# Performance work log

Hardware: AMD Instinct MI355X
Metric: run time of the kernel (lower is better)

The kernel has to match this reference:

```python
import jax, jax.numpy as jnp
import numpy as np


def _patches3x3(x):
    # x: [B,H,W,C] -> [B,H,W,9,C], SAME zero padding, patch index k = i*3+j
    B, H, W, C = x.shape
    p = jnp.pad(x, ((0, 0), (1, 1), (1, 1), (0, 0)))
    return jnp.stack([p[:, i:i + H, j:j + W, :] for i in range(3) for j in range(3)], axis=3)


def setup_inputs() -> dict:
    key = jax.random.key(0)
    k1, k2, k3 = jax.random.split(key, 3)
    B, H, W, CH, NC, DIM = 4, 80, 80, 256, 22, 256
    x = jax.random.normal(k1, (B, H, W, CH), dtype=jnp.float32)
    seg_mask = jax.random.uniform(k2, (B, H, W, NC), dtype=jnp.float32)
    # he_uniform over receptive field ch*3*3
    lim = np.sqrt(6.0 / (CH * 9)).astype(np.float32)
    conv_w = jax.random.uniform(k3, (CH, 3, 3, DIM), dtype=jnp.float32, minval=-lim, maxval=lim)
    return {"x": x, "seg_mask": seg_mask, "conv_w": conv_w}


def reference(x, seg_mask, conv_w):
    B, H, W, CH = x.shape
    NC = seg_mask.shape[-1]
    DIM = conv_w.shape[-1]
    # patches of segmentation map: [B,H,W,9,NC]
    s_patch = _patches3x3(seg_mask)
    m = seg_mask[:, :, :, None, :]                       # [B,H,W,1,NC]
    s_max = jnp.max(m, axis=-1, keepdims=True)           # [B,H,W,1,1]
    # keep patch values only for the argmax class at the center pixel
    sel = jnp.sum(jnp.where(m == s_max, s_patch, 0.0), axis=-1)  # [B,H,W,9]
    cnt = jnp.sum((sel != 0.0).astype(jnp.float32), axis=-1, keepdims=True)  # [B,H,W,1]
    norm = jnp.where(cnt > 0, 9.0 / jnp.maximum(cnt, 1.0), 0.0)  # divide_no_nan(9, cnt)
    # per-channel 3x3 patch extraction of features (== depthwise conv with eye(9))
    xp = _patches3x3(x)                                  # [B,H,W,9,CH]
    xp = xp * sel[..., None]                             # mask-gated patches
    w = conv_w.reshape(CH, 9, DIM)
    out = jnp.einsum('bhwkc,ckd->bhwd', xp, w) * norm    # [B,H,W,DIM]
    return out
```

## Files before the change

### kernel.cpp

```cpp
#include <hip/hip_runtime.h>
#include <hip/hip_bf16.h>
#include <cstdint>

#define B_ 4
#define H_ 80
#define W_ 80
#define CH_ 256
#define NC_ 22
#define DIM_ 256
#define NPIX (B_*H_*W_)

typedef __attribute__((ext_vector_type(8))) short short8;
typedef __attribute__((ext_vector_type(4))) float floatx4;

static __device__ inline unsigned short f2bf(float v) {
    __hip_bfloat16 h = __float2bfloat16(v);
    unsigned short r;
    __builtin_memcpy(&r, &h, 2);
    return r;
}

__global__ __launch_bounds__(256) void sel_kernel(const float* __restrict__ seg,
                                                  float* __restrict__ ssel)
{
    int m = blockIdx.x * 256 + threadIdx.x;
    if (m >= NPIX) return;
    int w = m % W_;
    int h = (m / W_) % H_;
    int b = m / (W_ * H_);

    const float2* c2 = (const float2*)(seg + (size_t)m * NC_);
    float cv[NC_];
    #pragma unroll
    for (int c = 0; c < NC_ / 2; ++c) { float2 v = c2[c]; cv[2*c] = v.x; cv[2*c+1] = v.y; }
    float mx = -1e30f;
    #pragma unroll
    for (int c = 0; c < NC_; ++c) mx = fmaxf(mx, cv[c]);

    float sel[9];
    int cnt = 0;
    #pragma unroll
    for (int k = 0; k < 9; ++k) {
        int i = k / 3, j = k % 3;
        int hh = h + i - 1, ww = w + j - 1;
        float s = 0.f;
        if (hh >= 0 && hh < H_ && ww >= 0 && ww < W_) {
            const float2* n2 = (const float2*)(seg + ((size_t)((b * H_ + hh) * W_ + ww)) * NC_);
            #pragma unroll
            for (int c = 0; c < NC_ / 2; ++c) {
                float2 v = n2[c];
                s += (cv[2*c]   == mx) ? v.x : 0.f;
                s += (cv[2*c+1] == mx) ? v.y : 0.f;
            }
        }
        sel[k] = s;
        cnt += (s != 0.f) ? 1 : 0;
    }
    float norm = (cnt > 0) ? 9.f / (float)cnt : 0.f;
    #pragma unroll
    for (int k = 0; k < 9; ++k)
        ssel[k * NPIX + m] = sel[k] * norm;
}

__global__ __launch_bounds__(256) void cvt_w_kernel(const float* __restrict__ cw,
                                                    unsigned short* __restrict__ wbT)
{
    int t = blockIdx.x * 256 + threadIdx.x;
    if (t >= 9 * 256 * 32) return;
    int c8 = t & 31;
    int d  = (t >> 5) & 255;
    int k  = t >> 13;
    unsigned int u[4];
    #pragma unroll
    for (int e = 0; e < 4; ++e) {
        float v0 = cw[(size_t)(c8*8 + 2*e    ) * 9 * DIM_ + k * DIM_ + d];
        float v1 = cw[(size_t)(c8*8 + 2*e + 1) * 9 * DIM_ + k * DIM_ + d];
        u[e] = (unsigned)f2bf(v0) | ((unsigned)f2bf(v1) << 16);
    }
    uint4* dst = (uint4*)(wbT + ((size_t)k * 256 + d) * 256 + c8 * 8);
    *dst = make_uint4(u[0], u[1], u[2], u[3]);
}

__global__ __launch_bounds__(256, 3) void conv_mfma(const float* __restrict__ x,
                                                    const float* __restrict__ ssel,
                                                    const unsigned short* __restrict__ wbT,
                                                    float* __restrict__ out)
{
    __shared__ __align__(16) unsigned short xsc[2][80][40];
    __shared__ __align__(16) unsigned short wl[2][128][40];
    __shared__ float sl[9][80];

    const int tid  = threadIdx.x;
    const int lane = tid & 63;
    const int wv   = tid >> 6;
    const int ln   = lane & 15;
    const int quad = lane >> 4;
    const int rt   = blockIdx.x;
    const int b    = rt / H_;
    const int h    = rt % H_;
    const int d0   = blockIdx.y * 128;

    const bool xact = tid < 160;
    const int  xtm  = tid >> 1;
    const int  xth  = tid & 1;
    const int  wtd  = tid >> 1;
    const int  wth  = tid & 1;

    for (int t = tid; t < 9 * 80; t += 256) {
        int k = t / 80, m = t - k * 80;
        sl[k][m] = ssel[k * NPIX + rt * W_ + m];
    }
    __syncthreads();

    floatx4 acc[5][2];
    #pragma unroll
    for (int i = 0; i < 5; ++i)
        #pragma unroll
        for (int j = 0; j < 2; ++j)
            acc[i][j] = (floatx4){0.f, 0.f, 0.f, 0.f};

    float4 xr0, xr1, xr2, xr3;
    float4 wr0, wr1;
    float  sc = 0.f;
    bool   xnz = false;

    auto stage1 = [&](int it) {
        const int k2  = it % 9;
        const int cc2 = (it / 9) * 32;
        const int i2  = k2 / 3;
        const int j2  = k2 - 3 * i2;
        const float4* q = (const float4*)(wbT + (((size_t)k2 * 256 + d0 + wtd) * 256
                                                 + cc2 + wth * 16));
        wr0 = q[0];
        wr1 = q[1];
        if (xact) {
            sc = sl[k2][xtm];
            const int r = h + i2 - 1;
            const int c = xtm + j2 - 1;
            xnz = (r >= 0) && (r < H_) && (c >= 0) && (c < W_);
            if (xnz) {
                const float4* p = (const float4*)(x + ((((size_t)b * H_ + r) * W_ + c) * CH_
                                                       + cc2 + xth * 16));
                xr0 = p[0]; xr1 = p[1]; xr2 = p[2]; xr3 = p[3];
            }
        }
    };

    auto stage2 = [&](int it) {
        const int buf = it & 1;
        float4* wd = (float4*)&wl[buf][wtd][wth * 16];
        wd[0] = wr0;
        wd[1] = wr1;
        if (xact) {
            unsigned int u[8];
            if (xnz) {
                float f[16] = {xr0.x, xr0.y, xr0.z, xr0.w, xr1.x, xr1.y, xr1.z, xr1.w,
                               xr2.x, xr2.y, xr2.z, xr2.w, xr3.x, xr3.y, xr3.z, xr3.w};
                #pragma unroll
                for (int e = 0; e < 8; ++e)
                    u[e] = (unsigned)f2bf(f[2*e] * sc) | ((unsigned)f2bf(f[2*e+1] * sc) << 16);
            } else {
                #pragma unroll
                for (int e = 0; e < 8; ++e) u[e] = 0u;
            }
            uint4* xd = (uint4*)&xsc[buf][xtm][xth * 16];
            xd[0] = make_uint4(u[0], u[1], u[2], u[3]);
            xd[1] = make_uint4(u[4], u[5], u[6], u[7]);
        }
    };

    stage1(0);
    stage2(0);
    __syncthreads();

    for (int it = 0; it < 72; ++it) {
        const int nit = it + 1;
        if (nit < 72) stage1(nit);

        const int buf = it & 1;
        short8 a[5];
        #pragma unroll
        for (int i = 0; i < 5; ++i)
            a[i] = *(const short8*)&xsc[buf][i * 16 + ln][quad * 8];
        short8 bb[2];
        #pragma unroll
        for (int j = 0; j < 2; ++j)
            bb[j] = *(const short8*)&wl[buf][wv * 32 + j * 16 + ln][quad * 8];
        #pragma unroll
        for (int i = 0; i < 5; ++i)
            #pragma unroll
            for (int j = 0; j < 2; ++j)
                acc[i][j] = __builtin_amdgcn_mfma_f32_16x16x32_bf16(a[i], bb[j], acc[i][j],
                                                                    0, 0, 0);

        if (nit < 72) stage2(nit);
        __syncthreads();
    }

    #pragma unroll
    for (int i = 0; i < 5; ++i) {
        #pragma unroll
        for (int j = 0; j < 2; ++j) {
            const int dd = d0 + wv * 32 + j * 16 + ln;
            #pragma unroll
            for (int r = 0; r < 4; ++r) {
                const int m = i * 16 + quad * 4 + r;
                out[((size_t)(rt * W_ + m)) * DIM_ + dd] = acc[i][j][r];
            }
        }
    }
}

extern "C" void kernel_launch(void* const* d_in, const int* in_sizes, int n_in,
                              void* d_out, int out_size, void* d_ws, size_t ws_size,
                              hipStream_t stream)
{
    const float* x   = (const float*)d_in[0];
    const float* seg = (const float*)d_in[1];
    const float* cw  = (const float*)d_in[2];
    float* out = (float*)d_out;

    float*          ssel = (float*)d_ws;
    unsigned short* wbT  = (unsigned short*)((char*)d_ws + 921600);

    sel_kernel<<<dim3((NPIX + 255) / 256), dim3(256), 0, stream>>>(seg, ssel);
    cvt_w_kernel<<<dim3(288), dim3(256), 0, stream>>>(cw, wbT);
    conv_mfma<<<dim3(B_ * H_, DIM_ / 128), dim3(256), 0, stream>>>(x, ssel, wbT, out);
}
```

Before: 173.6 us.

## Restructure conv GEMM with 128-channel K tiles, register B, and bf16 x precast

```diff
diff --git a/kernel.cpp b/kernel.cpp
--- a/kernel.cpp
+++ b/kernel.cpp
@@ -10,20 +10,24 @@
 #define DIM_ 256
 #define NPIX (B_*H_*W_)
 
+typedef unsigned short ushort;
 typedef __attribute__((ext_vector_type(8))) short short8;
 typedef __attribute__((ext_vector_type(4))) float floatx4;
 
-static __device__ inline unsigned short f2bf(float v) {
+static __device__ inline ushort f2bf(float v) {
     __hip_bfloat16 h = __float2bfloat16(v);
-    unsigned short r;
+    ushort r;
     __builtin_memcpy(&r, &h, 2);
     return r;
 }
-
-__global__ __launch_bounds__(256) void sel_kernel(const float* __restrict__ seg,
-                                                  float* __restrict__ ssel)
-{
-    int m = blockIdx.x * 256 + threadIdx.x;
+static __device__ inline unsigned pk2(float a, float b) {
+    return (unsigned)f2bf(a) | ((unsigned)f2bf(b) << 16);
+}
+
+__global__ __launch_bounds__(64) void sel_kernel(const float* __restrict__ seg,
+                                                 float* __restrict__ ssel)
+{
+    int m = blockIdx.x * 64 + threadIdx.x;
     if (m >= NPIX) return;
     int w = m % W_;
     int h = (m / W_) % H_;
@@ -62,33 +66,54 @@
         ssel[k * NPIX + m] = sel[k] * norm;
 }
 
-__global__ __launch_bounds__(256) void cvt_w_kernel(const float* __restrict__ cw,
-                                                    unsigned short* __restrict__ wbT)
-{
-    int t = blockIdx.x * 256 + threadIdx.x;
-    if (t >= 9 * 256 * 32) return;
-    int c8 = t & 31;
-    int d  = (t >> 5) & 255;
-    int k  = t >> 13;
-    unsigned int u[4];
-    #pragma unroll
-    for (int e = 0; e < 4; ++e) {
-        float v0 = cw[(size_t)(c8*8 + 2*e    ) * 9 * DIM_ + k * DIM_ + d];
-        float v1 = cw[(size_t)(c8*8 + 2*e + 1) * 9 * DIM_ + k * DIM_ + d];
-        u[e] = (unsigned)f2bf(v0) | ((unsigned)f2bf(v1) << 16);
-    }
-    uint4* dst = (uint4*)(wbT + ((size_t)k * 256 + d) * 256 + c8 * 8);
-    *dst = make_uint4(u[0], u[1], u[2], u[3]);
-}
-
-__global__ __launch_bounds__(256, 3) void conv_mfma(const float* __restrict__ x,
-                                                    const float* __restrict__ ssel,
-                                                    const unsigned short* __restrict__ wbT,
-                                                    float* __restrict__ out)
-{
-    __shared__ __align__(16) unsigned short xsc[2][80][40];
-    __shared__ __align__(16) unsigned short wl[2][128][40];
-    __shared__ float sl[9][80];
+__global__ __launch_bounds__(256) void cvt_w(const float* __restrict__ cw,
+                                             ushort* __restrict__ wbT)
+{
+    __shared__ ushort ls[32][260];
+    const int k  = blockIdx.x / 8;
+    const int c0 = (blockIdx.x % 8) * 32;
+    const int c   = threadIdx.x >> 3;
+    const int seg = threadIdx.x & 7;
+
+    const float* src = cw + ((size_t)(c0 + c) * 9 + k) * DIM_ + seg * 32;
+    #pragma unroll
+    for (int e = 0; e < 32; e += 4) {
+        float4 v = *(const float4*)(src + e);
+        unsigned* dst = (unsigned*)&ls[c][seg * 32 + e];
+        dst[0] = pk2(v.x, v.y);
+        dst[1] = pk2(v.z, v.w);
+    }
+    __syncthreads();
+
+    const int d = threadIdx.x;
+    ushort tmp[32];
+    #pragma unroll
+    for (int cc = 0; cc < 32; ++cc) tmp[cc] = ls[cc][d];
+    uint4 o[4];
+    __builtin_memcpy(o, tmp, 64);
+    uint4* dst = (uint4*)(wbT + ((size_t)k * 256 + d) * 256 + c0);
+    dst[0] = o[0]; dst[1] = o[1]; dst[2] = o[2]; dst[3] = o[3];
+}
+
+__global__ __launch_bounds__(256) void cvt_x(const float* __restrict__ x,
+                                             ushort* __restrict__ xb)
+{
+    size_t idx = ((size_t)blockIdx.x * 256 + threadIdx.x) * 8;
+    const float4* s = (const float4*)(x + idx);
+    float4 a = s[0], b = s[1];
+    uint4 o = make_uint4(pk2(a.x, a.y), pk2(a.z, a.w), pk2(b.x, b.y), pk2(b.z, b.w));
+    *(uint4*)(xb + idx) = o;
+}
+
+template<bool XB16>
+__global__ __launch_bounds__(256, 3) void conv2(const float* __restrict__ x,
+                                                const ushort* __restrict__ xb,
+                                                const float* __restrict__ ssel,
+                                                const ushort* __restrict__ wbT,
+                                                float* __restrict__ out)
+{
+    __shared__ ushort xsA[2][80 * 136];
+    __shared__ float  sl[9][80];
 
     const int tid  = threadIdx.x;
     const int lane = tid & 63;
@@ -100,112 +125,147 @@
     const int h    = rt % H_;
     const int d0   = blockIdx.y * 128;
 
-    const bool xact = tid < 160;
-    const int  xtm  = tid >> 1;
-    const int  xth  = tid & 1;
-    const int  wtd  = tid >> 1;
-    const int  wth  = tid & 1;
+    int qm[5], qc[5];
+    #pragma unroll
+    for (int r = 0; r < 5; ++r) {
+        int q = tid + 256 * r;
+        qm[r] = q >> 4;
+        qc[r] = q & 15;
+    }
 
     for (int t = tid; t < 9 * 80; t += 256) {
         int k = t / 80, m = t - k * 80;
         sl[k][m] = ssel[k * NPIX + rt * W_ + m];
     }
+
+    floatx4 O[5][2];
+    #pragma unroll
+    for (int i = 0; i < 5; ++i)
+        #pragma unroll
+        for (int jn = 0; jn < 2; ++jn)
+            O[i][jn] = (floatx4){0.f, 0.f, 0.f, 0.f};
+
+    uint4  sg[5];
+    float4 fa[5], fb[5];
+    bool   ok[5];
+
+    auto stage_load = [&](int nit) {
+        const int i   = nit / 6;
+        const int rem = nit % 6;
+        const int cc  = (rem / 3) * 128;
+        const int jj  = rem % 3;
+        const int rr  = h + i - 1;
+        const bool rowok = (rr >= 0) && (rr < H_);
+        const int rsafe = rowok ? rr : h;
+        #pragma unroll
+        for (int r = 0; r < 5; ++r) {
+            const int col = qm[r] + jj - 1;
+            const bool v = rowok && (col >= 0) && (col < W_);
+            ok[r] = v;
+            const size_t gp = ((size_t)(b * H_ + rsafe) * W_ + (v ? col : 0));
+            if (XB16) {
+                sg[r] = *(const uint4*)(xb + gp * CH_ + cc + qc[r] * 8);
+            } else {
+                const float* f = x + gp * CH_ + cc + qc[r] * 8;
+                fa[r] = *(const float4*)f;
+                fb[r] = *(const float4*)(f + 4);
+            }
+        }
+    };
+    auto stage_write = [&](int nit) {
+        ushort* bp = xsA[nit & 1];
+        #pragma unroll
+        for (int r = 0; r < 5; ++r) {
+            uint4 v;
+            if (XB16) {
+                v = ok[r] ? sg[r] : make_uint4(0u, 0u, 0u, 0u);
+            } else {
+                v = ok[r] ? make_uint4(pk2(fa[r].x, fa[r].y), pk2(fa[r].z, fa[r].w),
+                                       pk2(fb[r].x, fb[r].y), pk2(fb[r].z, fb[r].w))
+                          : make_uint4(0u, 0u, 0u, 0u);
+            }
+            *(uint4*)&bp[qm[r] * 136 + qc[r] * 8] = v;
+        }
+    };
+
+    short8 Breg[8];
+    auto loadB = [&](int nit) {
+        const int i   = nit / 6;
+        const int rem = nit % 6;
+        const int cc  = (rem / 3) * 128;
+        const int jj  = rem % 3;
+        const int k   = 3 * i + jj;
+        #pragma unroll
+        for (int kk = 0; kk < 4; ++kk)
+            #pragma unroll
+            for (int jn = 0; jn < 2; ++jn)
+                Breg[kk * 2 + jn] = *(const short8*)(wbT
+                    + ((size_t)k * 256 + d0 + wv * 32 + jn * 16 + ln) * 256
+                    + cc + kk * 32 + quad * 8);
+    };
+
+    stage_load(0);
+    stage_write(0);
+    loadB(0);
     __syncthreads();
 
-    floatx4 acc[5][2];
-    #pragma unroll
-    for (int i = 0; i < 5; ++i)
-        #pragma unroll
-        for (int j = 0; j < 2; ++j)
-            acc[i][j] = (floatx4){0.f, 0.f, 0.f, 0.f};
-
-    float4 xr0, xr1, xr2, xr3;
-    float4 wr0, wr1;
-    float  sc = 0.f;
-    bool   xnz = false;
-
-    auto stage1 = [&](int it) {
-        const int k2  = it % 9;
-        const int cc2 = (it / 9) * 32;
-        const int i2  = k2 / 3;
-        const int j2  = k2 - 3 * i2;
-        const float4* q = (const float4*)(wbT + (((size_t)k2 * 256 + d0 + wtd) * 256
-                                                 + cc2 + wth * 16));
-        wr0 = q[0];
-        wr1 = q[1];
-        if (xact) {
-            sc = sl[k2][xtm];
-            const int r = h + i2 - 1;
-            const int c = xtm + j2 - 1;
-            xnz = (r >= 0) && (r < H_) && (c >= 0) && (c < W_);
-            if (xnz) {
-                const float4* p = (const float4*)(x + ((((size_t)b * H_ + r) * W_ + c) * CH_
-                                                       + cc2 + xth * 16));
-                xr0 = p[0]; xr1 = p[1]; xr2 = p[2]; xr3 = p[3];
-            }
-        }
-    };
-
-    auto stage2 = [&](int it) {
-        const int buf = it & 1;
-        float4* wd = (float4*)&wl[buf][wtd][wth * 16];
-        wd[0] = wr0;
-        wd[1] = wr1;
-        if (xact) {
-            unsigned int u[8];
-            if (xnz) {
-                float f[16] = {xr0.x, xr0.y, xr0.z, xr0.w, xr1.x, xr1.y, xr1.z, xr1.w,
-                               xr2.x, xr2.y, xr2.z, xr2.w, xr3.x, xr3.y, xr3.z, xr3.w};
+    #pragma unroll 2
+    for (int it = 0; it < 18; ++it) {
+        const int i   = it / 6;
+        const int rem = it % 6;
+        const int jj  = rem % 3;
+        const int k   = 3 * i + jj;
+        const ushort* bp = xsA[it & 1];
+
+        if (it < 17) stage_load(it + 1);
+
+        floatx4 P[5][2];
+        #pragma unroll
+        for (int im = 0; im < 5; ++im)
+            #pragma unroll
+            for (int jn = 0; jn < 2; ++jn)
+                P[im][jn] = (floatx4){0.f, 0.f, 0.f, 0.f};
+
+        #pragma unroll
+        for (int kk = 0; kk < 4; ++kk) {
+            short8 a[5];
+            #pragma unroll
+            for (int im = 0; im < 5; ++im)
+                a[im] = *(const short8*)&bp[(im * 16 + ln) * 136 + kk * 32 + quad * 8];
+            #pragma unroll
+            for (int im = 0; im < 5; ++im)
                 #pragma unroll
-                for (int e = 0; e < 8; ++e)
-                    u[e] = (unsigned)f2bf(f[2*e] * sc) | ((unsigned)f2bf(f[2*e+1] * sc) << 16);
-            } else {
-                #pragma unroll
-                for (int e = 0; e < 8; ++e) u[e] = 0u;
-            }
-            uint4* xd = (uint4*)&xsc[buf][xtm][xth * 16];
-            xd[0] = make_uint4(u[0], u[1], u[2], u[3]);
-            xd[1] = make_uint4(u[4], u[5], u[6], u[7]);
-        }
-    };
-
-    stage1(0);
-    stage2(0);
-    __syncthreads();
-
-    for (int it = 0; it < 72; ++it) {
-        const int nit = it + 1;
-        if (nit < 72) stage1(nit);
-
-        const int buf = it & 1;
-        short8 a[5];
-        #pragma unroll
-        for (int i = 0; i < 5; ++i)
-            a[i] = *(const short8*)&xsc[buf][i * 16 + ln][quad * 8];
-        short8 bb[2];
-        #pragma unroll
-        for (int j = 0; j < 2; ++j)
-            bb[j] = *(const short8*)&wl[buf][wv * 32 + j * 16 + ln][quad * 8];
-        #pragma unroll
-        for (int i = 0; i < 5; ++i)
-            #pragma unroll
-            for (int j = 0; j < 2; ++j)
-                acc[i][j] = __builtin_amdgcn_mfma_f32_16x16x32_bf16(a[i], bb[j], acc[i][j],
-                                                                    0, 0, 0);
-
-        if (nit < 72) stage2(nit);
+                for (int jn = 0; jn < 2; ++jn)
+                    P[im][jn] = __builtin_amdgcn_mfma_f32_16x16x32_bf16(
+                        a[im], Breg[kk * 2 + jn], P[im][jn], 0, 0, 0);
+        }
+
+        if (it < 17) stage_write(it + 1);
+        if (it < 17) loadB(it + 1);
+
+        #pragma unroll
+        for (int im = 0; im < 5; ++im) {
+            const float4 sv = *(const float4*)&sl[k][im * 16 + quad * 4];
+            #pragma unroll
+            for (int jn = 0; jn < 2; ++jn) {
+                O[im][jn][0] += sv.x * P[im][jn][0];
+                O[im][jn][1] += sv.y * P[im][jn][1];
+                O[im][jn][2] += sv.z * P[im][jn][2];
+                O[im][jn][3] += sv.w * P[im][jn][3];
+            }
+        }
         __syncthreads();
     }
 
     #pragma unroll
-    for (int i = 0; i < 5; ++i) {
-        #pragma unroll
-        for (int j = 0; j < 2; ++j) {
-            const int dd = d0 + wv * 32 + j * 16 + ln;
+    for (int im = 0; im < 5; ++im) {
+        #pragma unroll
+        for (int jn = 0; jn < 2; ++jn) {
+            const int dd = d0 + wv * 32 + jn * 16 + ln;
             #pragma unroll
             for (int r = 0; r < 4; ++r) {
-                const int m = i * 16 + quad * 4 + r;
-                out[((size_t)(rt * W_ + m)) * DIM_ + dd] = acc[i][j][r];
+                const int m = im * 16 + quad * 4 + r;
+                out[((size_t)(rt * W_ + m)) * DIM_ + dd] = O[im][jn][r];
             }
         }
     }
@@ -220,10 +280,18 @@
     const float* cw  = (const float*)d_in[2];
     float* out = (float*)d_out;
 
-    float*          ssel = (float*)d_ws;
-    unsigned short* wbT  = (unsigned short*)((char*)d_ws + 921600);
-
-    sel_kernel<<<dim3((NPIX + 255) / 256), dim3(256), 0, stream>>>(seg, ssel);
-    cvt_w_kernel<<<dim3(288), dim3(256), 0, stream>>>(cw, wbT);
-    conv_mfma<<<dim3(B_ * H_, DIM_ / 128), dim3(256), 0, stream>>>(x, ssel, wbT, out);
-}
+    float*  ssel = (float*)d_ws;
+    ushort* wbT  = (ushort*)((char*)d_ws + 921600);
+    ushort* xb   = (ushort*)((char*)d_ws + 921600 + 1179648);
+    const size_t need = 921600u + 1179648u + 13107200u;
+
+    sel_kernel<<<dim3((NPIX + 63) / 64), dim3(64), 0, stream>>>(seg, ssel);
+    cvt_w<<<dim3(72), dim3(256), 0, stream>>>(cw, wbT);
+
+    if (ws_size >= need) {
+        cvt_x<<<dim3(NPIX * CH_ / (256 * 8)), dim3(256), 0, stream>>>(x, xb);
+        conv2<true><<<dim3(B_ * H_, 2), dim3(256), 0, stream>>>(x, xb, ssel, wbT, out);
+    } else {
+        conv2<false><<<dim3(B_ * H_, 2), dim3(256), 0, stream>>>(x, nullptr, ssel, wbT, out);
+    }
+}
```

Result: faster. 158.2 us (-8.9%).
